# Kernel tuning notes

Measured on AMD Instinct MI355X. Metric: run time of the kernel, lower is better.

## Reference

```python
import jax, jax.numpy as jnp
import numpy as np

D = 2524
EXP = 4
EPS = 1e-8

def _rmsnorm(x, scale):
    # p=-1 default: full RMSNorm, rms = ||x||_2 / sqrt(d)
    rms = jnp.sqrt(jnp.sum(x * x, axis=-1, keepdims=True)) * (D ** -0.5)
    return scale * (x / (rms + EPS))

def setup_inputs() -> dict:
    key = jax.random.key(0)
    ks = jax.random.split(key, 16)
    S, B = 512, 32
    H = EXP * D
    s = 0.02
    return {
        'x': jax.random.normal(ks[0], (S, B, D), jnp.float32),
        'y': jax.random.normal(ks[1], (S, B), jnp.float32),
        'mask': jnp.ones((B, S), jnp.float32),
        'norm1_scale': jnp.ones((D,), jnp.float32),
        'norm2_scale': jnp.ones((D,), jnp.float32),
        'w1': jax.random.normal(ks[2], (H, D), jnp.float32) * s,
        'b1': jnp.zeros((H,), jnp.float32),
        'w2': jax.random.normal(ks[3], (D, H), jnp.float32) * s,
        'b2': jnp.zeros((D,), jnp.float32),
        'att_w': jax.random.normal(ks[4], (D, D), jnp.float32) * s,
        'att_b': jnp.zeros((D,), jnp.float32),
        'lin_w': jax.random.normal(ks[5], (D, D), jnp.float32) * s,
        'lin_b': jnp.zeros((D,), jnp.float32),
        'fc_w': jax.random.normal(ks[6], (6, D), jnp.float32) * s,
        'fc_b': jnp.zeros((6,), jnp.float32),
    }

def reference(x, y, mask, norm1_scale, norm2_scale, w1, b1, w2, b2,
              att_w, att_b, lin_w, lin_b, fc_w, fc_b):
    # x: (S, B, D); mask: (B, S)
    residual = x
    x = jnp.fft.fft2(x, axes=(-1, -2)).real                 # FNet token/feature mixing
    x = _rmsnorm(x + residual, norm1_scale)
    residual = x
    h = jax.nn.gelu(x @ w1.T + b1, approximate=False)       # (S,B,4D), dropout=identity (eval)
    x = h @ w2.T + b2
    emotions = _rmsnorm(x + residual, norm2_scale)           # (S,B,D)

    # MatchingAttention 'general2', vectorized over all query positions t
    q = emotions @ att_w.T + att_b                           # (S,B,D)
    Mm = emotions * mask.T[:, :, None]                       # mask memory: (S,B,D)
    scores = jnp.einsum('tbd,sbd->bts', q, Mm) * mask[:, None, :]
    a = jax.nn.softmax(jnp.tanh(scores), axis=-1)
    a = a * mask[:, None, :]
    a = a / jnp.sum(a, axis=-1, keepdims=True)               # (B,T,S)
    att_emotions = jnp.einsum('bts,sbd->tbd', a, emotions)   # (S,B,D)
    alpha = jnp.transpose(a, (1, 0, 2))                      # (T,B,S): stacked alpha_[:,0,:]

    hidden = jax.nn.relu(att_emotions @ lin_w.T + lin_b)     # (S,B,D)
    log_prob = hidden @ fc_w.T + fc_b                        # (S,B,6)
    return (log_prob, alpha)
```

## Files before the change

### kernel.cpp

```cpp
#include <hip/hip_runtime.h>
#include <hip/hip_bf16.h>
#include <math.h>

#define SLEN 512
#define BATCH 32
#define DIM 2524
#define DK 2560
#define NTOK 16384
#define LD1 2560
#define LDH 5120

using f32x4 = __attribute__((ext_vector_type(4))) float;
using bfrag = __attribute__((ext_vector_type(8))) short;

__device__ __forceinline__ short f2bs(float f) {
  __hip_bfloat16 h = __float2bfloat16(f);
  return *reinterpret_cast<short*>(&h);
}
__device__ __forceinline__ float bs2f(short s) {
  __hip_bfloat16 h;
  *reinterpret_cast<short*>(&h) = s;
  return __bfloat162float(h);
}

__device__ __forceinline__ void gload16(const short* g, short* l) {
  __builtin_amdgcn_global_load_lds(
      (const __attribute__((address_space(1))) void*)g,
      (__attribute__((address_space(3))) void*)l, 16, 0, 0);
}

__global__ void k_conv_pad(const float* __restrict__ in, short* __restrict__ out,
                           int Min, int Kin, int Mout, int Kout, int roff, int coff) {
  const int cpr = Kout >> 2;
  long idx = (long)blockIdx.x * 256 + threadIdx.x;
  if (idx >= (long)Mout * cpr) return;
  int r = (int)(idx / cpr);
  int c4 = (int)(idx % cpr) * 4;
  short4 o;
#pragma unroll
  for (int j = 0; j < 4; j++) {
    int c = c4 + j;
    float v = (roff + r < Min && coff + c < Kin) ? in[(long)(roff + r) * Kin + coff + c] : 0.f;
    ((short*)&o)[j] = f2bs(v);
  }
  *(short4*)(out + (long)r * Kout + c4) = o;
}

__global__ void k_gen_cs2(short* __restrict__ out) {
  const int cpr = LDH >> 2;
  long idx = (long)blockIdx.x * 256 + threadIdx.x;
  if (idx >= (long)LD1 * cpr) return;
  int r = (int)(idx / cpr);
  int c4 = (int)(idx % cpr) * 4;
  short4 o;
#pragma unroll
  for (int j = 0; j < 4; j++) {
    int c = c4 + j;
    float v = 0.f;
    if (r < DIM) {
      if (c < DIM) {
        int mm = (c * r) % DIM;
        v = cosf((float)mm * (6.2831853071795864f / (float)DIM));
      } else if (c >= LD1 && c < LD1 + DIM) {
        int mm = ((c - LD1) * r) % DIM;
        v = -sinf((float)mm * (6.2831853071795864f / (float)DIM));
      }
    }
    ((short*)&o)[j] = f2bs(v);
  }
  *(short4*)(out + (long)r * LDH + c4) = o;
}

__global__ __launch_bounds__(256) void k_bmix1(const float* __restrict__ x,
                                               short* __restrict__ xri) {
  __shared__ float xs[32][64];
  __shared__ float tc[32][32];
  __shared__ float ts[32][32];
  const int s = blockIdx.x;
  const int d0 = blockIdx.y * 64;
  const int tid = threadIdx.x;
  for (int j = tid; j < 1024; j += 256) {
    int bp = j >> 5, b = j & 31;
    float th = (float)((b * bp) & 31) * (6.2831853071795864f / 32.f);
    tc[bp][b] = cosf(th);
    ts[bp][b] = sinf(th);
  }
#pragma unroll
  for (int j = 0; j < 8; j++) {
    int lin = j * 256 + tid;
    int b = lin >> 6, dd = lin & 63;
    int d = d0 + dd;
    xs[b][dd] = (d < DIM) ? x[((long)s * 32 + b) * DIM + d] : 0.f;
  }
  __syncthreads();
  const int g = tid >> 6, dd = tid & 63;
  const int d = d0 + dd;
  const bool ok = d < DIM;
#pragma unroll
  for (int j = 0; j < 8; j++) {
    int bp = g * 8 + j;
    float P = 0.f, Q = 0.f;
#pragma unroll
    for (int b = 0; b < 32; b++) {
      float v = xs[b][dd];
      P += v * tc[bp][b];
      Q += v * ts[bp][b];
    }
    long row = (long)s * 32 + bp;
    xri[row * LDH + d] = ok ? f2bs(P) : (short)0;
    xri[row * LDH + LD1 + d] = ok ? f2bs(Q) : (short)0;
  }
}

__global__ __launch_bounds__(512, 2) void gemm256(
    const short* __restrict__ A, long lda,
    const short* __restrict__ Bt, long ldb,
    void* __restrict__ Cout, long ldc,
    int N, int nzero, int K,
    const float* __restrict__ bias,
    const float* __restrict__ res, long ldres,
    int gn, int epi) {
  __shared__ __align__(16) short lds[65536];
  const int tid = threadIdx.x;
  const int w = tid >> 6;
  const int l = tid & 63;
  const int nwg = gridDim.x;
  const int lin = blockIdx.x;
  const int swz = (lin & 7) * (nwg >> 3) + (lin >> 3);
  const int bm = swz / gn, bn = swz % gn;
  const long row0 = (long)bm * 256;
  const long col0 = (long)bn * 256;
  const int wm = w >> 2, wn = w & 3;
  const short* Ab = A + row0 * lda;
  const short* Bb = Bt + col0 * ldb;
  const int rloc = l & 15;
  const int kslot = l >> 4;
  const int kloc = ((w & 1) * 4 + kslot) * 8;
  const int sblk = w >> 1;
  const int sdst = (w & 1) * 512;

  f32x4 acc[8][4] = {};
  bfrag af[4][2], bf0[2][2], bf1[2][2];
  const int nt = K >> 6;

#define STAGE(bufbit, isB, h, s, kt)                                          \
  {                                                                           \
    const short* gsrc = ((isB) ? Bb : Ab) +                                   \
        (long)((h) * 128 + ((s) * 4 + sblk) * 16 + rloc) * ((isB) ? ldb : lda) + \
        (long)(kt) * 64 + kloc;                                               \
    short* ldst = &lds[(bufbit) * 32768 + (isB) * 16384 + (h) * 8192 +        \
                       ((s) * 4 + sblk) * 1024 + sdst];                       \
    gload16(gsrc, ldst);                                                      \
  }
#define LDAF(buf, i, ks) \
  (*(const bfrag*)&lds[(buf) * 32768 + (wm * 8 + (i)) * 1024 + ((ks) * 4 + kslot) * 128 + rloc * 8])
#define LDBF(buf, j, ks) \
  (*(const bfrag*)&lds[(buf) * 32768 + 16384 + (wn * 4 + (j)) * 1024 + ((ks) * 4 + kslot) * 128 + rloc * 8])

  STAGE(0, 0, 0, 0, 0) STAGE(0, 0, 0, 1, 0) STAGE(0, 1, 0, 0, 0) STAGE(0, 1, 0, 1, 0)
  STAGE(0, 0, 1, 0, 0) STAGE(0, 0, 1, 1, 0) STAGE(0, 1, 1, 0, 0) STAGE(0, 1, 1, 1, 0)
  STAGE(1, 0, 0, 0, 1) STAGE(1, 0, 0, 1, 1) STAGE(1, 1, 0, 0, 1) STAGE(1, 1, 0, 1, 1)
  STAGE(1, 0, 1, 0, 1) STAGE(1, 0, 1, 1, 1) STAGE(1, 1, 1, 0, 1) STAGE(1, 1, 1, 1, 1)
  asm volatile("s_waitcnt vmcnt(8)" ::: "memory");
  __builtin_amdgcn_s_barrier();

  for (int t = 0; t < nt; ++t) {
    const int cur = t & 1;
    const int kt2 = (t + 2 < nt) ? t + 2 : nt - 1;
#pragma unroll
    for (int i = 0; i < 4; i++) { af[i][0] = LDAF(cur, i, 0); af[i][1] = LDAF(cur, i, 1); }
#pragma unroll
    for (int j = 0; j < 2; j++) { bf0[j][0] = LDBF(cur, j, 0); bf0[j][1] = LDBF(cur, j, 1); }
    asm volatile("s_waitcnt lgkmcnt(0)" ::: "memory");
    __builtin_amdgcn_sched_barrier(0);
    __builtin_amdgcn_s_setprio(1);
#pragma unroll
    for (int ks = 0; ks < 2; ks++)
#pragma unroll
      for (int i = 0; i < 4; i++)
#pragma unroll
        for (int j = 0; j < 2; j++)
          acc[i][j] = __builtin_amdgcn_mfma_f32_16x16x32_bf16(af[i][ks], bf0[j][ks], acc[i][j], 0, 0, 0);
    __builtin_amdgcn_s_setprio(0);
    __builtin_amdgcn_s_barrier();
#pragma unroll
    for (int i = 0; i < 4; i++) { af[i][0] = LDAF(cur, 4 + i, 0); af[i][1] = LDAF(cur, 4 + i, 1); }
    asm volatile("s_waitcnt lgkmcnt(0)" ::: "memory");
    __builtin_amdgcn_sched_barrier(0);
    __builtin_amdgcn_s_setprio(1);
#pragma unroll
    for (int ks = 0; ks < 2; ks++)
#pragma unroll
      for (int i = 0; i < 4; i++)
#pragma unroll
        for (int j = 0; j < 2; j++)
          acc[4 + i][j] = __builtin_amdgcn_mfma_f32_16x16x32_bf16(af[i][ks], bf0[j][ks], acc[4 + i][j], 0, 0, 0);
    __builtin_amdgcn_s_setprio(0);
    __builtin_amdgcn_s_barrier();
#pragma unroll
    for (int j = 0; j < 2; j++) { bf1[j][0] = LDBF(cur, 2 + j, 0); bf1[j][1] = LDBF(cur, 2 + j, 1); }
    asm volatile("s_waitcnt lgkmcnt(0)" ::: "memory");
    __builtin_amdgcn_sched_barrier(0);
    __builtin_amdgcn_s_setprio(1);
#pragma unroll
    for (int ks = 0; ks < 2; ks++)
#pragma unroll
      for (int i = 0; i < 4; i++)
#pragma unroll
        for (int j = 0; j < 2; j++)
          acc[4 + i][2 + j] = __builtin_amdgcn_mfma_f32_16x16x32_bf16(af[i][ks], bf1[j][ks], acc[4 + i][2 + j], 0, 0, 0);
    __builtin_amdgcn_s_setprio(0);
    __builtin_amdgcn_s_barrier();
#pragma unroll
    for (int i = 0; i < 4; i++) { af[i][0] = LDAF(cur, i, 0); af[i][1] = LDAF(cur, i, 1); }
    asm volatile("s_waitcnt lgkmcnt(0)" ::: "memory");
    __builtin_amdgcn_sched_barrier(0);
    __builtin_amdgcn_s_barrier();
    STAGE(cur, 0, 0, 0, kt2) STAGE(cur, 0, 0, 1, kt2)
    STAGE(cur, 1, 0, 0, kt2) STAGE(cur, 1, 0, 1, kt2)
    STAGE(cur, 0, 1, 0, kt2) STAGE(cur, 0, 1, 1, kt2)
    STAGE(cur, 1, 1, 0, kt2) STAGE(cur, 1, 1, 1, kt2)
    __builtin_amdgcn_sched_barrier(0);
    __builtin_amdgcn_s_setprio(1);
#pragma unroll
    for (int ks = 0; ks < 2; ks++)
#pragma unroll
      for (int i = 0; i < 4; i++)
#pragma unroll
        for (int j = 0; j < 2; j++)
          acc[i][2 + j] = __builtin_amdgcn_mfma_f32_16x16x32_bf16(af[i][ks], bf1[j][ks], acc[i][2 + j], 0, 0, 0);
    __builtin_amdgcn_s_setprio(0);
    asm volatile("s_waitcnt vmcnt(8)" ::: "memory");
    __builtin_amdgcn_s_barrier();
  }
  asm volatile("s_waitcnt vmcnt(0)" ::: "memory");

  float* outF = (float*)Cout;
  __hip_bfloat16* outB = (__hip_bfloat16*)Cout;
  const int erow = kslot * 4;
  const int ecol = rloc;
#pragma unroll
  for (int i = 0; i < 8; i++) {
#pragma unroll
    for (int e = 0; e < 4; e++) {
      long grow = row0 + wm * 128 + i * 16 + erow + e;
#pragma unroll
      for (int j = 0; j < 4; j++) {
        int gcol = (int)col0 + wn * 64 + j * 16 + ecol;
        if (gcol >= nzero) continue;
        float v = 0.f;
        if (gcol < N) {
          v = acc[i][j][e];
          if (bias) v += bias[gcol];
          if (epi == 1) v += res[grow * ldres + gcol];
          else if (epi == 2) v = 0.5f * v * (1.f + erff(v * 0.70710678118f));
          else if (epi == 4) v = fmaxf(v, 0.f);
        }
        if (epi == 6) outF[grow * ldc + gcol] += v;
        else if (epi <= 1) outF[grow * ldc + gcol] = v;
        else outB[grow * ldc + gcol] = __float2bfloat16(v);
      }
    }
  }
#undef STAGE
#undef LDAF
#undef LDBF
}

__global__ __launch_bounds__(256) void gemm_bt(
    const short* __restrict__ A, long sA, long lda,
    const short* __restrict__ Bt, long sB, long ldb,
    void* __restrict__ Cout, long sC, long ldc,
    int N, int nzero, int K,
    const float* __restrict__ bias,
    const float* __restrict__ mask, long sMask,
    int epi) {
  __shared__ __align__(16) short As[4096];
  __shared__ __align__(16) short Bs[4096];
  const int tid = threadIdx.x;
  const int wave = tid >> 6;
  const int lane = tid & 63;
  const int z = blockIdx.z;
  const long row0 = (long)blockIdx.x * 128;
  const long col0 = (long)blockIdx.y * 128;
  const int wm = wave >> 1, wn = wave & 1;
  const short* Ab = A + z * sA + row0 * lda;
  const short* Bb = Bt + z * sB + col0 * ldb;
  const int r0 = tid >> 2, c0 = (tid & 3) * 8;
  const int r1 = r0 + 64;
  short* dA0 = As + (wave << 9);
  short* dA1 = As + 2048 + (wave << 9);
  short* dB0 = Bs + (wave << 9);
  short* dB1 = Bs + 2048 + (wave << 9);
  f32x4 acc[4][4] = {};
  for (int k0 = 0; k0 < K; k0 += 32) {
    __syncthreads();
    gload16(Ab + (long)r0 * lda + k0 + c0, dA0);
    gload16(Ab + (long)r1 * lda + k0 + c0, dA1);
    gload16(Bb + (long)r0 * ldb + k0 + c0, dB0);
    gload16(Bb + (long)r1 * ldb + k0 + c0, dB1);
    __syncthreads();
    const int kb = (lane >> 4) << 3;
    const int rr = lane & 15;
    bfrag a[4], b[4];
#pragma unroll
    for (int i = 0; i < 4; i++)
      a[i] = *(const bfrag*)&As[(wm * 64 + i * 16 + rr) * 32 + kb];
#pragma unroll
    for (int j = 0; j < 4; j++)
      b[j] = *(const bfrag*)&Bs[(wn * 64 + j * 16 + rr) * 32 + kb];
#pragma unroll
    for (int i = 0; i < 4; i++)
#pragma unroll
      for (int j = 0; j < 4; j++)
        acc[i][j] = __builtin_amdgcn_mfma_f32_16x16x32_bf16(a[i], b[j], acc[i][j], 0, 0, 0);
  }
  float* outF = (float*)Cout + z * sC;
  __hip_bfloat16* outB = (__hip_bfloat16*)Cout + z * sC;
  const float* mz = mask ? mask + z * sMask : nullptr;
  const int erow = (lane >> 4) * 4;
  const int ecol = lane & 15;
#pragma unroll
  for (int i = 0; i < 4; i++) {
#pragma unroll
    for (int e = 0; e < 4; e++) {
      long grow = row0 + wm * 64 + i * 16 + erow + e;
#pragma unroll
      for (int j = 0; j < 4; j++) {
        int gcol = (int)col0 + wn * 64 + j * 16 + ecol;
        if (gcol >= nzero) continue;
        float v = 0.f;
        if (gcol < N) {
          v = acc[i][j][e];
          if (bias) v += bias[gcol];
          if (epi == 5) v = tanhf(v * mz[gcol]);
        }
        if (epi == 5) outF[grow * ldc + gcol] = v;
        else outB[grow * ldc + gcol] = __float2bfloat16(v);
      }
    }
  }
}

__global__ __launch_bounds__(256) void k_rms(const float* __restrict__ in, long ldin,
                                             const float* __restrict__ scale,
                                             float* __restrict__ outf,
                                             short* __restrict__ outb1,
                                             short* __restrict__ outb2,
                                             const float* __restrict__ mask) {
  const long row = blockIdx.x;
  const float* rp = in + row * ldin;
  const int tid = threadIdx.x;
  float ss = 0.f;
  for (int d = tid; d < DIM; d += 256) { float v = rp[d]; ss = fmaf(v, v, ss); }
  __shared__ float red[4];
  for (int o = 32; o; o >>= 1) ss += __shfl_down(ss, o);
  if ((tid & 63) == 0) red[tid >> 6] = ss;
  __syncthreads();
  float tot = red[0] + red[1] + red[2] + red[3];
  float rms = sqrtf(tot * (1.f / (float)DIM));
  float inv = 1.f / (rms + 1e-8f);
  float mf = 1.f;
  if (mask) mf = mask[(row & 31) * SLEN + (int)(row >> 5)];
  for (int d = tid; d < DK; d += 256) {
    float v = (d < DIM) ? rp[d] * inv * scale[d] : 0.f;
    if (outf) outf[row * DK + d] = v;
    if (outb1) outb1[row * DK + d] = f2bs(v);
    if (outb2) outb2[row * DK + d] = f2bs(v * mf);
  }
}

__global__ __launch_bounds__(256) void k_transpose(const short* __restrict__ emob,
                                                   short* __restrict__ emoT) {
  __shared__ short t[64][66];
  const int b = blockIdx.z;
  const int d0 = blockIdx.y * 64;
  const int s0 = blockIdx.x * 64;
  const int tid = threadIdx.x;
#pragma unroll
  for (int j = 0; j < 16; j++) {
    int lin = j * 256 + tid;
    int r = lin >> 6, c = lin & 63;
    int d = d0 + c;
    t[r][c] = (d < DIM) ? emob[((long)(s0 + r) * 32 + b) * DK + d] : (short)0;
  }
  __syncthreads();
#pragma unroll
  for (int j = 0; j < 16; j++) {
    int lin = j * 256 + tid;
    int r = lin >> 6, c = lin & 63;
    emoT[((long)b * 2560 + d0 + r) * SLEN + s0 + c] = t[c][r];
  }
}

__global__ __launch_bounds__(256) void k_softmax(const float* __restrict__ sc,
                                                 const float* __restrict__ mask,
                                                 float* __restrict__ alpha,
                                                 short* __restrict__ ab) {
  const int r = blockIdx.x;
  const int b = r >> 9, tq = r & 511;
  const float* row = sc + (long)r * SLEN;
  const int tid = threadIdx.x;
  const int lane = tid & 63, wv = tid >> 6;
  __shared__ float red[4];
  float v0 = row[tid], v1 = row[tid + 256];
  float m = fmaxf(v0, v1);
  for (int o = 32; o; o >>= 1) m = fmaxf(m, __shfl_down(m, o));
  if (lane == 0) red[wv] = m;
  __syncthreads();
  m = fmaxf(fmaxf(red[0], red[1]), fmaxf(red[2], red[3]));
  __syncthreads();
  float e0 = expf(v0 - m), e1 = expf(v1 - m);
  float s = e0 + e1;
  for (int o = 32; o; o >>= 1) s += __shfl_down(s, o);
  if (lane == 0) red[wv] = s;
  __syncthreads();
  s = red[0] + red[1] + red[2] + red[3];
  __syncthreads();
  float m0 = mask[b * SLEN + tid], m1 = mask[b * SLEN + tid + 256];
  float a0 = e0 / s * m0, a1 = e1 / s * m1;
  float s2 = a0 + a1;
  for (int o = 32; o; o >>= 1) s2 += __shfl_down(s2, o);
  if (lane == 0) red[wv] = s2;
  __syncthreads();
  s2 = red[0] + red[1] + red[2] + red[3];
  float f0 = a0 / s2, f1 = a1 / s2;
  long ob = ((long)tq * BATCH + b) * SLEN;
  alpha[ob + tid] = f0;
  alpha[ob + tid + 256] = f1;
  ab[(long)r * SLEN + tid] = f2bs(f0);
  ab[(long)r * SLEN + tid + 256] = f2bs(f1);
}

__global__ __launch_bounds__(256) void k_logprob(const short* __restrict__ hid,
                                                 const float* __restrict__ fcw,
                                                 const float* __restrict__ fcb,
                                                 float* __restrict__ out) {
  const int tok = blockIdx.x * 4 + (threadIdx.x >> 6);
  const int lane = threadIdx.x & 63;
  const short* hr = hid + (long)tok * DK;
  float p0 = 0, p1 = 0, p2 = 0, p3 = 0, p4 = 0, p5 = 0;
  for (int d = lane; d < DIM; d += 64) {
    float h = bs2f(hr[d]);
    p0 += h * fcw[d];
    p1 += h * fcw[DIM + d];
    p2 += h * fcw[2 * DIM + d];
    p3 += h * fcw[3 * DIM + d];
    p4 += h * fcw[4 * DIM + d];
    p5 += h * fcw[5 * DIM + d];
  }
  for (int o = 32; o; o >>= 1) {
    p0 += __shfl_down(p0, o); p1 += __shfl_down(p1, o); p2 += __shfl_down(p2, o);
    p3 += __shfl_down(p3, o); p4 += __shfl_down(p4, o); p5 += __shfl_down(p5, o);
  }
  if (lane == 0) {
    float* o6 = out + (long)tok * 6;
    o6[0] = p0 + fcb[0]; o6[1] = p1 + fcb[1]; o6[2] = p2 + fcb[2];
    o6[3] = p3 + fcb[3]; o6[4] = p4 + fcb[4]; o6[5] = p5 + fcb[5];
  }
}

extern "C" void kernel_launch(void* const* d_in, const int* in_sizes, int n_in,
                              void* d_out, int out_size, void* d_ws, size_t ws_size,
                              hipStream_t stream) {
  const float* x    = (const float*)d_in[0];
  const float* mask = (const float*)d_in[2];
  const float* n1s  = (const float*)d_in[3];
  const float* n2s  = (const float*)d_in[4];
  const float* w1   = (const float*)d_in[5];
  const float* b1   = (const float*)d_in[6];
  const float* w2   = (const float*)d_in[7];
  const float* b2   = (const float*)d_in[8];
  const float* attw = (const float*)d_in[9];
  const float* att_bias = (const float*)d_in[10];
  const float* linw = (const float*)d_in[11];
  const float* lin_bias = (const float*)d_in[12];
  const float* fcw  = (const float*)d_in[13];
  const float* fcb  = (const float*)d_in[14];
  float* out = (float*)d_out;

  const size_t R2 = 0;
  const size_t R3 = 167772160;
  const size_t R4 = 335544320;
  const size_t RF = 419430400;
  const size_t TOTAL = 445644800;
  if (ws_size < TOTAL) return;

  char* ws = (char*)d_ws;
  float* t1   = (float*)(ws + R2);
  short* hbH  = (short*)(ws + R2);
  short* emob = (short*)(ws + R2);
  short* mmb  = (short*)(ws + R2 + 83886080);
  float* scr  = (float*)(ws + R2);
  short* ab   = (short*)(ws + R2 + 33554432);
  short* xri  = (short*)(ws + R3);
  float* x1f  = (float*)(ws + R3);
  float* t2   = x1f;
  short* atb  = (short*)(ws + R3);
  short* emoT = (short*)(ws + R3 + 83886080);
  short* x1b  = (short*)(ws + R4);
  short* qb   = (short*)(ws + R4);
  short* hidb = (short*)(ws + R4);
  short* wtb  = (short*)(ws + RF);

  dim3 blk(256), blk5(512);
  k_bmix1<<<dim3(512, 40), blk, 0, stream>>>(x, xri);
  k_gen_cs2<<<dim3((LD1 * (LDH / 4) + 255) / 256), blk, 0, stream>>>(wtb);
  gemm256<<<dim3(640), blk5, 0, stream>>>(xri, LDH, wtb, LDH, t1, LD1,
                                          DIM, 2560, LDH, nullptr, x, DIM, 10, 1);
  k_rms<<<dim3(NTOK), blk, 0, stream>>>(t1, LD1, n1s, x1f, x1b, nullptr, nullptr);
  k_conv_pad<<<dim3((5120 * 640 + 255) / 256), blk, 0, stream>>>(w1, wtb, 10096, 2524, 5120, 2560, 0, 0);
  gemm256<<<dim3(1280), blk5, 0, stream>>>(x1b, DK, wtb, DK, hbH, LDH,
                                           5120, 5120, DK, b1, nullptr, 0, 20, 2);
  k_conv_pad<<<dim3((2560 * 1280 + 255) / 256), blk, 0, stream>>>(w2, wtb, 2524, 10096, 2560, 5120, 0, 0);
  gemm256<<<dim3(640), blk5, 0, stream>>>(hbH, LDH, wtb, LDH, t2, DK,
                                          DIM, 2560, LDH, b2, x1f, DK, 10, 1);
  k_conv_pad<<<dim3((5120 * 640 + 255) / 256), blk, 0, stream>>>(w1, wtb, 10096, 2524, 5120, 2560, 5120, 0);
  gemm256<<<dim3(1280), blk5, 0, stream>>>(x1b, DK, wtb, DK, hbH, LDH,
                                           4976, 5120, DK, b1 + 5120, nullptr, 0, 20, 2);
  k_conv_pad<<<dim3((2560 * 1280 + 255) / 256), blk, 0, stream>>>(w2, wtb, 2524, 10096, 2560, 5120, 0, 5120);
  gemm256<<<dim3(640), blk5, 0, stream>>>(hbH, LDH, wtb, LDH, t2, DK,
                                          2560, 2560, LDH, nullptr, nullptr, 0, 10, 6);
  k_rms<<<dim3(NTOK), blk, 0, stream>>>(t2, DK, n2s, nullptr, emob, mmb, mask);
  k_transpose<<<dim3(8, 40, 32), blk, 0, stream>>>(emob, emoT);
  k_conv_pad<<<dim3((2560 * 640 + 255) / 256), blk, 0, stream>>>(attw, wtb, 2524, 2524, 2560, 2560, 0, 0);
  gemm256<<<dim3(640), blk5, 0, stream>>>(emob, DK, wtb, DK, qb, DK,
                                          DIM, 2560, DK, att_bias, nullptr, 0, 10, 3);
  gemm_bt<<<dim3(4, 4, 32), blk, 0, stream>>>(qb, DK, (long)BATCH * DK, mmb, DK, (long)BATCH * DK,
                                              scr, (long)SLEN * SLEN, SLEN,
                                              SLEN, SLEN, DK, nullptr, mask, SLEN, 5);
  k_softmax<<<dim3(NTOK), blk, 0, stream>>>(scr, mask, out + 98304, ab);
  gemm_bt<<<dim3(4, 20, 32), blk, 0, stream>>>(ab, (long)SLEN * SLEN, SLEN, emoT, (long)2560 * SLEN, SLEN,
                                               atb, DK, (long)BATCH * DK,
                                               2560, 2560, SLEN, nullptr, nullptr, 0, 3);
  k_conv_pad<<<dim3((2560 * 640 + 255) / 256), blk, 0, stream>>>(linw, wtb, 2524, 2524, 2560, 2560, 0, 0);
  gemm256<<<dim3(640), blk5, 0, stream>>>(atb, DK, wtb, DK, hidb, DK,
                                          DIM, 2560, DK, lin_bias, nullptr, 0, 10, 4);
  k_logprob<<<dim3(NTOK / 4), blk, 0, stream>>>(hidb, fcw, fcb, out);
}
```

Measured before the change: 5.793 ms.

## Restructure big GEMM mainloop to k-half phases with interleaved next-tile prefetch

The 256x256 GEMM mainloop changes from a prefetch-distance-2 scheme, where all next loads were issued in one burst late in the iteration, to a double-buffered scheme. Loads for the next k-tile are split into four quarter-stages interleaved with the four MFMA phases. The LDS layout is reorganised by k-half (ks), so each phase loads one 32-wide k slice of A and B fragments and runs 16 MFMAs. This spreads global-to-LDS traffic across the iteration and cuts fragment register use, but shortens prefetch distance to one tile and adds barriers.

```diff
diff --git a/kernel.cpp b/kernel.cpp
--- a/kernel.cpp
+++ b/kernel.cpp
@@ -135,102 +135,101 @@
   const short* Bb = Bt + col0 * ldb;
   const int rloc = l & 15;
   const int kslot = l >> 4;
-  const int kloc = ((w & 1) * 4 + kslot) * 8;
-  const int sblk = w >> 1;
-  const int sdst = (w & 1) * 512;
 
   f32x4 acc[8][4] = {};
-  bfrag af[4][2], bf0[2][2], bf1[2][2];
+  bfrag af[4], bf[4];
   const int nt = K >> 6;
 
-#define STAGE(bufbit, isB, h, s, kt)                                          \
-  {                                                                           \
-    const short* gsrc = ((isB) ? Bb : Ab) +                                   \
-        (long)((h) * 128 + ((s) * 4 + sblk) * 16 + rloc) * ((isB) ? ldb : lda) + \
-        (long)(kt) * 64 + kloc;                                               \
-    short* ldst = &lds[(bufbit) * 32768 + (isB) * 16384 + (h) * 8192 +        \
-                       ((s) * 4 + sblk) * 1024 + sdst];                       \
-    gload16(gsrc, ldst);                                                      \
+#define STAGEA(bufbit, ks, L, kt)                                              \
+  {                                                                            \
+    const short* gsrc = Ab + (long)(((L) * 8 + w) * 16 + rloc) * lda +         \
+                        (long)(kt) * 64 + (ks) * 32 + kslot * 8;               \
+    short* ldst = &lds[(bufbit) * 32768 + (ks) * 8192 + ((L) * 8 + w) * 512];  \
+    gload16(gsrc, ldst);                                                       \
+  }
+#define STAGEB(bufbit, ks, L, kt)                                              \
+  {                                                                            \
+    const short* gsrc = Bb + (long)(((L) * 8 + w) * 16 + rloc) * ldb +         \
+                        (long)(kt) * 64 + (ks) * 32 + kslot * 8;               \
+    short* ldst = &lds[(bufbit) * 32768 + 16384 + (ks) * 8192 + ((L) * 8 + w) * 512]; \
+    gload16(gsrc, ldst);                                                       \
   }
 #define LDAF(buf, i, ks) \
-  (*(const bfrag*)&lds[(buf) * 32768 + (wm * 8 + (i)) * 1024 + ((ks) * 4 + kslot) * 128 + rloc * 8])
+  (*(const bfrag*)&lds[(buf) * 32768 + (ks) * 8192 + (wm * 8 + (i)) * 512 + kslot * 128 + rloc * 8])
 #define LDBF(buf, j, ks) \
-  (*(const bfrag*)&lds[(buf) * 32768 + 16384 + (wn * 4 + (j)) * 1024 + ((ks) * 4 + kslot) * 128 + rloc * 8])
-
-  STAGE(0, 0, 0, 0, 0) STAGE(0, 0, 0, 1, 0) STAGE(0, 1, 0, 0, 0) STAGE(0, 1, 0, 1, 0)
-  STAGE(0, 0, 1, 0, 0) STAGE(0, 0, 1, 1, 0) STAGE(0, 1, 1, 0, 0) STAGE(0, 1, 1, 1, 0)
-  STAGE(1, 0, 0, 0, 1) STAGE(1, 0, 0, 1, 1) STAGE(1, 1, 0, 0, 1) STAGE(1, 1, 0, 1, 1)
-  STAGE(1, 0, 1, 0, 1) STAGE(1, 0, 1, 1, 1) STAGE(1, 1, 1, 0, 1) STAGE(1, 1, 1, 1, 1)
-  asm volatile("s_waitcnt vmcnt(8)" ::: "memory");
+  (*(const bfrag*)&lds[(buf) * 32768 + 16384 + (ks) * 8192 + (wn * 4 + (j)) * 512 + kslot * 128 + rloc * 8])
+
+  STAGEA(0, 0, 0, 0) STAGEA(0, 0, 1, 0)
+  STAGEB(0, 0, 0, 0) STAGEB(0, 0, 1, 0)
+  STAGEA(0, 1, 0, 0) STAGEA(0, 1, 1, 0)
+  STAGEB(0, 1, 0, 0) STAGEB(0, 1, 1, 0)
+  asm volatile("s_waitcnt vmcnt(4)" ::: "memory");
   __builtin_amdgcn_s_barrier();
 
   for (int t = 0; t < nt; ++t) {
-    const int cur = t & 1;
-    const int kt2 = (t + 2 < nt) ? t + 2 : nt - 1;
-#pragma unroll
-    for (int i = 0; i < 4; i++) { af[i][0] = LDAF(cur, i, 0); af[i][1] = LDAF(cur, i, 1); }
-#pragma unroll
-    for (int j = 0; j < 2; j++) { bf0[j][0] = LDBF(cur, j, 0); bf0[j][1] = LDBF(cur, j, 1); }
+    const int cur = t & 1, nb = cur ^ 1;
+    const int ktn = (t + 1 < nt) ? t + 1 : t;
+#pragma unroll
+    for (int i = 0; i < 4; i++) af[i] = LDAF(cur, i, 0);
+#pragma unroll
+    for (int j = 0; j < 4; j++) bf[j] = LDBF(cur, j, 0);
+    STAGEA(nb, 0, 0, ktn) STAGEA(nb, 0, 1, ktn)
+    __builtin_amdgcn_s_barrier();
     asm volatile("s_waitcnt lgkmcnt(0)" ::: "memory");
     __builtin_amdgcn_sched_barrier(0);
     __builtin_amdgcn_s_setprio(1);
 #pragma unroll
-    for (int ks = 0; ks < 2; ks++)
-#pragma unroll
-      for (int i = 0; i < 4; i++)
-#pragma unroll
-        for (int j = 0; j < 2; j++)
-          acc[i][j] = __builtin_amdgcn_mfma_f32_16x16x32_bf16(af[i][ks], bf0[j][ks], acc[i][j], 0, 0, 0);
+    for (int i = 0; i < 4; i++)
+#pragma unroll
+      for (int j = 0; j < 4; j++)
+        acc[i][j] = __builtin_amdgcn_mfma_f32_16x16x32_bf16(af[i], bf[j], acc[i][j], 0, 0, 0);
     __builtin_amdgcn_s_setprio(0);
     __builtin_amdgcn_s_barrier();
 #pragma unroll
-    for (int i = 0; i < 4; i++) { af[i][0] = LDAF(cur, 4 + i, 0); af[i][1] = LDAF(cur, 4 + i, 1); }
+    for (int i = 0; i < 4; i++) af[i] = LDAF(cur, 4 + i, 0);
+    STAGEB(nb, 0, 0, ktn) STAGEB(nb, 0, 1, ktn)
+    __builtin_amdgcn_s_barrier();
     asm volatile("s_waitcnt lgkmcnt(0)" ::: "memory");
     __builtin_amdgcn_sched_barrier(0);
     __builtin_amdgcn_s_setprio(1);
 #pragma unroll
-    for (int ks = 0; ks < 2; ks++)
-#pragma unroll
-      for (int i = 0; i < 4; i++)
-#pragma unroll
-        for (int j = 0; j < 2; j++)
-          acc[4 + i][j] = __builtin_amdgcn_mfma_f32_16x16x32_bf16(af[i][ks], bf0[j][ks], acc[4 + i][j], 0, 0, 0);
+    for (int i = 0; i < 4; i++)
+#pragma unroll
+      for (int j = 0; j < 4; j++)
+        acc[4 + i][j] = __builtin_amdgcn_mfma_f32_16x16x32_bf16(af[i], bf[j], acc[4 + i][j], 0, 0, 0);
     __builtin_amdgcn_s_setprio(0);
-    __builtin_amdgcn_s_barrier();
-#pragma unroll
-    for (int j = 0; j < 2; j++) { bf1[j][0] = LDBF(cur, 2 + j, 0); bf1[j][1] = LDBF(cur, 2 + j, 1); }
+    asm volatile("s_waitcnt vmcnt(4)" ::: "memory");
+    __builtin_amdgcn_s_barrier();
+#pragma unroll
+    for (int i = 0; i < 4; i++) af[i] = LDAF(cur, i, 1);
+#pragma unroll
+    for (int j = 0; j < 4; j++) bf[j] = LDBF(cur, j, 1);
+    STAGEA(nb, 1, 0, ktn) STAGEA(nb, 1, 1, ktn)
+    __builtin_amdgcn_s_barrier();
     asm volatile("s_waitcnt lgkmcnt(0)" ::: "memory");
     __builtin_amdgcn_sched_barrier(0);
     __builtin_amdgcn_s_setprio(1);
 #pragma unroll
-    for (int ks = 0; ks < 2; ks++)
-#pragma unroll
-      for (int i = 0; i < 4; i++)
-#pragma unroll
-        for (int j = 0; j < 2; j++)
-          acc[4 + i][2 + j] = __builtin_amdgcn_mfma_f32_16x16x32_bf16(af[i][ks], bf1[j][ks], acc[4 + i][2 + j], 0, 0, 0);
+    for (int i = 0; i < 4; i++)
+#pragma unroll
+      for (int j = 0; j < 4; j++)
+        acc[i][j] = __builtin_amdgcn_mfma_f32_16x16x32_bf16(af[i], bf[j], acc[i][j], 0, 0, 0);
     __builtin_amdgcn_s_setprio(0);
     __builtin_amdgcn_s_barrier();
 #pragma unroll
-    for (int i = 0; i < 4; i++) { af[i][0] = LDAF(cur, i, 0); af[i][1] = LDAF(cur, i, 1); }
+    for (int i = 0; i < 4; i++) af[i] = LDAF(cur, 4 + i, 1);
+    STAGEB(nb, 1, 0, ktn) STAGEB(nb, 1, 1, ktn)
+    __builtin_amdgcn_s_barrier();
     asm volatile("s_waitcnt lgkmcnt(0)" ::: "memory");
     __builtin_amdgcn_sched_barrier(0);
-    __builtin_amdgcn_s_barrier();
-    STAGE(cur, 0, 0, 0, kt2) STAGE(cur, 0, 0, 1, kt2)
-    STAGE(cur, 1, 0, 0, kt2) STAGE(cur, 1, 0, 1, kt2)
-    STAGE(cur, 0, 1, 0, kt2) STAGE(cur, 0, 1, 1, kt2)
-    STAGE(cur, 1, 1, 0, kt2) STAGE(cur, 1, 1, 1, kt2)
-    __builtin_amdgcn_sched_barrier(0);
     __builtin_amdgcn_s_setprio(1);
 #pragma unroll
-    for (int ks = 0; ks < 2; ks++)
-#pragma unroll
-      for (int i = 0; i < 4; i++)
-#pragma unroll
-        for (int j = 0; j < 2; j++)
-          acc[i][2 + j] = __builtin_amdgcn_mfma_f32_16x16x32_bf16(af[i][ks], bf1[j][ks], acc[i][2 + j], 0, 0, 0);
+    for (int i = 0; i < 4; i++)
+#pragma unroll
+      for (int j = 0; j < 4; j++)
+        acc[4 + i][j] = __builtin_amdgcn_mfma_f32_16x16x32_bf16(af[i], bf[j], acc[4 + i][j], 0, 0, 0);
     __builtin_amdgcn_s_setprio(0);
-    asm volatile("s_waitcnt vmcnt(8)" ::: "memory");
+    asm volatile("s_waitcnt vmcnt(4)" ::: "memory");
     __builtin_amdgcn_s_barrier();
   }
   asm volatile("s_waitcnt vmcnt(0)" ::: "memory");
@@ -262,7 +261,8 @@
       }
     }
   }
-#undef STAGE
+#undef STAGEA
+#undef STAGEB
 #undef LDAF
 #undef LDBF
 }
```

Result: faster. 5.037 ms (-13.1%).
